# Kernel optimization log

Measured on AMD Instinct MI355X. Metric: run time of the kernel, lower is better.

Reference implementation:

```python
import jax, jax.numpy as jnp
import numpy as np

H = 64        # hidden_size
G = 64        # global_hidden_size
VOCAB = 128   # VOCAB_SIZE
NUM_OPS = 20
DEPTH = 12    # complete binary tree: 2**DEPTH - 1 nodes
B = 128       # batch of trees
TEMP = 3.0    # self.temperature


def setup_inputs() -> dict:
    key = jax.random.key(0)
    ks = jax.random.split(key, 16)
    s = 0.05
    N = 2 ** DEPTH - 1
    inp = {
        "x_idx": jax.random.randint(ks[0], (B, N), 0, VOCAB, dtype=jnp.int32),
        "validity_mask": jnp.ones((NUM_OPS,), jnp.float32),
        # binary tree-LSTM (blstm): x one-hot -> gates [i, f_a, f_b, o, u]
        "Wx": jax.random.normal(ks[1], (VOCAB, 5 * H), jnp.float32) * s,
        "Ua": jax.random.normal(ks[2], (H, 5 * H), jnp.float32) * s,
        "Ub": jax.random.normal(ks[3], (H, 5 * H), jnp.float32) * s,
        "b_tree": jnp.zeros((5 * H,), jnp.float32),
        # global nn.LSTM (1 layer), gate order i,f,g,o
        "W_ih": jax.random.normal(ks[4], (H, 4 * G), jnp.float32) * s,
        "W_hh": jax.random.normal(ks[5], (G, 4 * G), jnp.float32) * s,
        "b_lstm": jnp.zeros((4 * G,), jnp.float32),
        # FFN on root hidden
        "W1": jax.random.normal(ks[6], (H, H), jnp.float32) * s,
        "b1": jnp.zeros((H,), jnp.float32),
        "W2": jax.random.normal(ks[7], (H, H), jnp.float32) * s,
        "b2": jnp.zeros((H,), jnp.float32),
        # actor head on [hidden ; global_hidden]
        "actor_W": jax.random.normal(ks[8], (H + G, NUM_OPS), jnp.float32) * s,
        "actor_b": jnp.zeros((NUM_OPS,), jnp.float32),
    }
    return inp


def _tree_lstm_sweep(x_idx, Wx, Ua, Ub, b_tree):
    """Bottom-up binary tree-LSTM over a complete binary tree.
    Node i's children sit at flat positions 2i+1, 2i+2 (level layout)."""
    h_prev = c_prev = None
    for d in range(DEPTH - 1, -1, -1):
        n = 2 ** d
        off = n - 1
        # memory-bound gather of gate pre-activations: [B, n, 5H]
        z = Wx[x_idx[:, off:off + n]] + b_tree
        if h_prev is not None:
            h_a, h_b = h_prev[:, 0::2], h_prev[:, 1::2]
            c_a, c_b = c_prev[:, 0::2], c_prev[:, 1::2]
            z = z + jnp.einsum("bnh,hg->bng", h_a, Ua) + jnp.einsum("bnh,hg->bng", h_b, Ub)
        i, fa, fb, o, u = jnp.split(z, 5, axis=-1)
        c = jax.nn.sigmoid(i) * jnp.tanh(u)
        if h_prev is not None:
            c = c + jax.nn.sigmoid(fa) * c_a + jax.nn.sigmoid(fb) * c_b
        h = jax.nn.sigmoid(o) * jnp.tanh(c)
        h_prev, c_prev = h, c
    return h_prev[:, 0]  # root hidden [B, H]


def reference(x_idx, validity_mask, Wx, Ua, Ub, b_tree, W_ih, W_hh, b_lstm,
              W1, b1, W2, b2, actor_W, actor_b):
    h_root = _tree_lstm_sweep(x_idx, Wx, Ua, Ub, b_tree)
    # internal op 1: apply_ffn then apply_global_lstm
    f = jnp.maximum(h_root @ W1 + b1, 0.0) @ W2 + b2          # FFN [B, H]
    h0 = jnp.zeros((f.shape[0], G), f.dtype)
    g = f @ W_ih + h0 @ W_hh + b_lstm                          # one LSTM step
    i, fg, gg, o = jnp.split(g, 4, axis=-1)                    # torch order i,f,g,o
    c_g = jax.nn.sigmoid(i) * jnp.tanh(gg)                     # c0 = 0
    h_g = jax.nn.sigmoid(o) * jnp.tanh(c_g)                    # [B, G]
    # external actor with validity-masked weights (as in policy())
    feats = jnp.concatenate([f, h_g], axis=-1)                 # [B, H+G]
    logits = jnp.log(validity_mask) + feats @ (actor_W * validity_mask) + actor_b * validity_mask
    return jax.nn.softmax(logits / TEMP, axis=-1)              # [B, NUM_OPS]
```

## Files before the change

kernel.cpp:

```cpp
#include <hip/hip_runtime.h>


typedef unsigned short u16;
typedef unsigned int   u32;
typedef __attribute__((ext_vector_type(8))) short  short8;
typedef __attribute__((ext_vector_type(4))) float  floatx4;

__device__ __forceinline__ float fsig(float x) {
    return __fdividef(1.0f, 1.0f + __expf(-x));
}
__device__ __forceinline__ float ftanh(float x) {
    return 1.0f - __fdividef(2.0f, __expf(2.0f * x) + 1.0f);
}
__device__ __forceinline__ u16 f2bf(float x) {
    u32 u = __float_as_uint(x);
    return (u16)((u + 0x7FFFu + ((u >> 16) & 1u)) >> 16);
}
__device__ __forceinline__ float bf2f(short s) {
    return __uint_as_float(((u32)(u16)s) << 16);
}
__device__ __forceinline__ float c_from_slots(short lo, short hi) {
    return __uint_as_float((u32)(u16)lo | (((u32)(u16)hi) << 16));
}

#define HS 72
#define CS 65

__global__ void precompute_kernel(
    const float* __restrict__ Wx, const float* __restrict__ b_tree,
    const float* __restrict__ Ua, const float* __restrict__ Ub,
    u16* __restrict__ Wp, u16* __restrict__ Tap, u16* __restrict__ Tbp,
    u16* __restrict__ Uswz)
{
    int v = blockIdx.x;
    int t = threadIdx.x;
    __shared__ float sz[320], sta[320], stb[320], sh[64], sc[64];
    float z = Wx[v * 320 + t] + b_tree[t];
    sz[t] = z;
    {
        int f = v * 320 + t;
        int j = f & 7, lane = (f >> 3) & 63, tk = f >> 9;
        int nt = tk % 20, kc = tk / 20;
        int k = kc * 32 + (lane >> 4) * 8 + j;
        int nn = nt * 16 + (lane & 15);
        float uval = (k < 64) ? Ua[k * 320 + nn] : Ub[(k - 64) * 320 + nn];
        Uswz[f] = f2bf(uval);
    }
    __syncthreads();
    if (t < 64) {
        float c = fsig(sz[t]) * ftanh(sz[256 + t]);
        float h = fsig(sz[192 + t]) * ftanh(c);
        sc[t] = c; sh[t] = h;
    }
    __syncthreads();
    float ta = 0.f, tb = 0.f;
    #pragma unroll
    for (int k = 0; k < 64; ++k) {
        ta += sh[k] * Ua[k * 320 + t];
        tb += sh[k] * Ub[k * 320 + t];
    }
    sta[t] = ta; stb[t] = tb;
    __syncthreads();
    if (t < 64) {
        int hh = t;
        u32 cbits = __float_as_uint(sc[hh]);
        short8 wp, tp, bp;
        #pragma unroll
        for (int g = 0; g < 5; ++g) {
            wp[g] = (short)f2bf(sz[g * 64 + hh]);
            tp[g] = (short)f2bf(sta[g * 64 + hh]);
            bp[g] = (short)f2bf(stb[g * 64 + hh]);
        }
        wp[5] = 0; wp[6] = 0; wp[7] = 0;
        tp[5] = (short)(cbits & 0xFFFF); tp[6] = (short)(cbits >> 16); tp[7] = 0;
        bp[5] = tp[5]; bp[6] = tp[6]; bp[7] = 0;
        *(short8*)(Wp  + ((size_t)v * 64 + hh) * 8) = wp;
        *(short8*)(Tap + ((size_t)v * 64 + hh) * 8) = tp;
        *(short8*)(Tbp + ((size_t)v * 64 + hh) * 8) = bp;
    }
}

template<int MT>
__device__ __forceinline__ void sweep_level(
    const u16* hsrc, const float* csrc,
    u16* hdst, float* cdst,
    u16* hg, float* cg,
    float* hroot,
    const short8 Bfrag[4][5],
    const u16* __restrict__ Wp, const int* __restrict__ xb,
    int nrows, int i0, int loff,
    int lane15, int quad, int wv)
{
    floatx4 acc[MT][5];
    #pragma unroll
    for (int mt = 0; mt < MT; ++mt)
        #pragma unroll
        for (int g = 0; g < 5; ++g) acc[mt][g] = (floatx4){0.f, 0.f, 0.f, 0.f};

    #pragma unroll
    for (int mt = 0; mt < MT; ++mt) {
        #pragma unroll
        for (int kc = 0; kc < 4; ++kc) {
            int child = 2 * (mt * 16 + lane15) + (kc >> 1);
            short8 a = *(const short8*)(hsrc + child * HS + (kc & 1) * 32 + quad * 8);
            #pragma unroll
            for (int g = 0; g < 5; ++g)
                acc[mt][g] = __builtin_amdgcn_mfma_f32_16x16x32_bf16(
                    a, Bfrag[kc][g], acc[mt][g], 0, 0, 0);
        }
    }

    int hh = wv * 16 + lane15;
    #pragma unroll
    for (int mt = 0; mt < MT; ++mt) {
        #pragma unroll
        for (int r = 0; r < 4; ++r) {
            int row = mt * 16 + quad * 4 + r;
            bool valid = row < nrows;
            int id = xb[loff + i0 + row];
            short8 wp = *(const short8*)(Wp + (((size_t)id << 6) + hh) * 8);
            float zi  = acc[mt][0][r] + bf2f(wp[0]);
            float zfa = acc[mt][1][r] + bf2f(wp[1]);
            float zfb = acc[mt][2][r] + bf2f(wp[2]);
            float zo  = acc[mt][3][r] + bf2f(wp[3]);
            float zu  = acc[mt][4][r] + bf2f(wp[4]);
            float ca = csrc[(2 * row) * CS + hh];
            float cb = csrc[(2 * row + 1) * CS + hh];
            float c = fsig(zi) * ftanh(zu) + fsig(zfa) * ca + fsig(zfb) * cb;
            float h = fsig(zo) * ftanh(c);
            if (valid) {
                if (hdst)  { hdst[row * HS + hh] = f2bf(h); cdst[row * CS + hh] = c; }
                if (hg)    { hg[row * 64 + hh] = f2bf(h);   cg[row * 64 + hh] = c; }
                if (hroot) { hroot[hh] = h; }
            }
        }
    }
}

__device__ __forceinline__ void load_bfrags(short8 Bfrag[4][5],
                                            const u16* __restrict__ Uswz,
                                            int wv, int lane)
{
    #pragma unroll
    for (int kc = 0; kc < 4; ++kc)
        #pragma unroll
        for (int g = 0; g < 5; ++g) {
            int nt = g * 4 + wv;
            Bfrag[kc][g] = *(const short8*)(Uswz + ((kc * 20 + nt) * 64 + lane) * 8);
        }
}

__global__ __launch_bounds__(256, 2) void sweepA_kernel(
    const int* __restrict__ x_idx,
    const u16* __restrict__ Wp, const u16* __restrict__ Tap,
    const u16* __restrict__ Tbp, const u16* __restrict__ Uswz,
    u16* __restrict__ h4, float* __restrict__ c4)
{
    __shared__ u16   hA[64 * HS];
    __shared__ u16   hB[32 * HS];
    __shared__ float cA[64 * CS];
    __shared__ float cB[32 * CS];
    int t = threadIdx.x, lane = t & 63, wv = t >> 6;
    int lane15 = lane & 15, quad = lane >> 4;
    int b = blockIdx.x >> 4, st = blockIdx.x & 15;
    const int* xb = x_idx + b * 4095;

    short8 Bfrag[4][5];
    load_bfrags(Bfrag, Uswz, wv, lane);

    #pragma unroll 2
    for (int rr = 0; rr < 16; ++rr) {
        int rl = wv * 16 + rr;
        int i = st * 64 + rl;
        int id  = xb[1023 + i];
        int ida = xb[2047 + 2 * i];
        int idb = xb[2048 + 2 * i];
        short8 wp = *(const short8*)(Wp  + (((size_t)id)  << 9) + lane * 8);
        short8 ta = *(const short8*)(Tap + (((size_t)ida) << 9) + lane * 8);
        short8 tb = *(const short8*)(Tbp + (((size_t)idb) << 9) + lane * 8);
        float zi  = bf2f(wp[0]) + bf2f(ta[0]) + bf2f(tb[0]);
        float zfa = bf2f(wp[1]) + bf2f(ta[1]) + bf2f(tb[1]);
        float zfb = bf2f(wp[2]) + bf2f(ta[2]) + bf2f(tb[2]);
        float zo  = bf2f(wp[3]) + bf2f(ta[3]) + bf2f(tb[3]);
        float zu  = bf2f(wp[4]) + bf2f(ta[4]) + bf2f(tb[4]);
        float ca = c_from_slots(ta[5], ta[6]);
        float cb = c_from_slots(tb[5], tb[6]);
        float c = fsig(zi) * ftanh(zu) + fsig(zfa) * ca + fsig(zfb) * cb;
        float h = fsig(zo) * ftanh(c);
        hA[rl * HS + lane] = f2bf(h);
        cA[rl * CS + lane] = c;
    }
    __syncthreads();
    sweep_level<2>(hA, cA, hB, cB, nullptr, nullptr, nullptr, Bfrag, Wp, xb,
                   32, st << 5, 511, lane15, quad, wv);
    __syncthreads();
    sweep_level<1>(hB, cB, hA, cA, nullptr, nullptr, nullptr, Bfrag, Wp, xb,
                   16, st << 4, 255, lane15, quad, wv);
    __syncthreads();
    sweep_level<1>(hA, cA, hB, cB, nullptr, nullptr, nullptr, Bfrag, Wp, xb,
                   8, st << 3, 127, lane15, quad, wv);
    __syncthreads();
    sweep_level<1>(hB, cB, hA, cA, nullptr, nullptr, nullptr, Bfrag, Wp, xb,
                   4, st << 2, 63, lane15, quad, wv);
    __syncthreads();
    sweep_level<1>(hA, cA, hB, cB, nullptr, nullptr, nullptr, Bfrag, Wp, xb,
                   2, st << 1, 31, lane15, quad, wv);
    __syncthreads();
    sweep_level<1>(hB, cB, nullptr, nullptr,
                   h4 + (size_t)(b * 16 + st) * 64, c4 + (size_t)(b * 16 + st) * 64,
                   nullptr, Bfrag, Wp, xb, 1, st, 15, lane15, quad, wv);
}

__global__ __launch_bounds__(256, 2) void sweepB_kernel(
    const int* __restrict__ x_idx,
    const u16* __restrict__ Wp, const u16* __restrict__ Uswz,
    const u16* __restrict__ h4, const float* __restrict__ c4,
    const float* __restrict__ W1, const float* __restrict__ b1,
    const float* __restrict__ W2, const float* __restrict__ b2,
    const float* __restrict__ W_ih, const float* __restrict__ b_lstm,
    const float* __restrict__ actor_W, const float* __restrict__ actor_b,
    const float* __restrict__ vm, float* __restrict__ out)
{
    __shared__ u16   hA[32 * HS];
    __shared__ u16   hB[32 * HS];
    __shared__ float cA[32 * CS];
    __shared__ float cB[32 * CS];
    __shared__ float hroot[64];
    int t = threadIdx.x, lane = t & 63, wv = t >> 6;
    int lane15 = lane & 15, quad = lane >> 4;
    int b = blockIdx.x;
    const int* xb = x_idx + b * 4095;

    short8 Bfrag[4][5];
    load_bfrags(Bfrag, Uswz, wv, lane);

    for (int idx = t; idx < 16 * 64; idx += 256) {
        int r = idx >> 6, hh = idx & 63;
        hA[r * HS + hh] = h4[(size_t)(b * 16 + r) * 64 + hh];
        cA[r * CS + hh] = c4[(size_t)(b * 16 + r) * 64 + hh];
    }
    __syncthreads();
    sweep_level<1>(hA, cA, hB, cB, nullptr, nullptr, nullptr, Bfrag, Wp, xb,
                   8, 0, 7, lane15, quad, wv);
    __syncthreads();
    sweep_level<1>(hB, cB, hA, cA, nullptr, nullptr, nullptr, Bfrag, Wp, xb,
                   4, 0, 3, lane15, quad, wv);
    __syncthreads();
    sweep_level<1>(hA, cA, hB, cB, nullptr, nullptr, nullptr, Bfrag, Wp, xb,
                   2, 0, 1, lane15, quad, wv);
    __syncthreads();
    sweep_level<1>(hB, cB, nullptr, nullptr, nullptr, nullptr, hroot, Bfrag, Wp, xb,
                   1, 0, 0, lane15, quad, wv);
    __syncthreads();

    if (wv == 0) {
        float a = b1[lane];
        #pragma unroll 8
        for (int k = 0; k < 64; ++k) a += hroot[k] * W1[k * 64 + lane];
        float r1 = fmaxf(a, 0.f);
        float f = b2[lane];
        #pragma unroll 8
        for (int k = 0; k < 64; ++k) f += __shfl(r1, k) * W2[k * 64 + lane];
        float gi = b_lstm[lane], gg = b_lstm[128 + lane], go = b_lstm[192 + lane];
        #pragma unroll 8
        for (int k = 0; k < 64; ++k) {
            float fk = __shfl(f, k);
            gi += fk * W_ih[k * 256 + lane];
            gg += fk * W_ih[k * 256 + 128 + lane];
            go += fk * W_ih[k * 256 + 192 + lane];
        }
        float cg = fsig(gi) * ftanh(gg);
        float hg = fsig(go) * ftanh(cg);
        int tt = (lane < 20) ? lane : 19;
        float dot = 0.f;
        #pragma unroll 8
        for (int k = 0; k < 64; ++k) {
            float fk = __shfl(f, k), hk = __shfl(hg, k);
            dot += fk * actor_W[k * 20 + tt] + hk * actor_W[(64 + k) * 20 + tt];
        }
        float m = vm[tt];
        float lg = logf(m) + dot * m + actor_b[tt] * m;
        float mx = -1e30f;
        #pragma unroll
        for (int j = 0; j < 20; ++j) mx = fmaxf(mx, __shfl(lg, j));
        float s = 0.f;
        #pragma unroll
        for (int j = 0; j < 20; ++j) s += __expf((__shfl(lg, j) - mx) * (1.0f / 3.0f));
        if (lane < 20) out[b * 20 + lane] = __expf((lg - mx) * (1.0f / 3.0f)) / s;
    }
}

extern "C" void kernel_launch(void* const* d_in, const int* in_sizes, int n_in,
                              void* d_out, int out_size, void* d_ws, size_t ws_size,
                              hipStream_t stream)
{
    const int*   x_idx   = (const int*)d_in[0];
    const float* vm      = (const float*)d_in[1];
    const float* Wx      = (const float*)d_in[2];
    const float* Ua      = (const float*)d_in[3];
    const float* Ub      = (const float*)d_in[4];
    const float* b_tree  = (const float*)d_in[5];
    const float* W_ih    = (const float*)d_in[6];
    const float* b_lstm  = (const float*)d_in[8];
    const float* W1      = (const float*)d_in[9];
    const float* b1      = (const float*)d_in[10];
    const float* W2      = (const float*)d_in[11];
    const float* b2      = (const float*)d_in[12];
    const float* actor_W = (const float*)d_in[13];
    const float* actor_b = (const float*)d_in[14];
    float* out = (float*)d_out;

    float* ws = (float*)d_ws;
    float* c4 = ws;  ws += 2048 * 64;
    u16* u = (u16*)ws;
    u16* Wp   = u;  u += 128 * 64 * 8;
    u16* Tap  = u;  u += 128 * 64 * 8;
    u16* Tbp  = u;  u += 128 * 64 * 8;
    u16* Uswz = u;  u += 128 * 320;
    u16* h4   = u;  u += 2048 * 64;

    precompute_kernel<<<128, 320, 0, stream>>>(Wx, b_tree, Ua, Ub,
                                               Wp, Tap, Tbp, Uswz);
    sweepA_kernel<<<2048, 256, 0, stream>>>(x_idx, Wp, Tap, Tbp, Uswz, h4, c4);
    sweepB_kernel<<<128, 256, 0, stream>>>(x_idx, Wp, Uswz, h4, c4,
                                           W1, b1, W2, b2, W_ih, b_lstm,
                                           actor_W, actor_b, vm, out);
}
```

Before: 183.5 us.

## Rebalance tree sweep split, store cell state in bf16 pairs, use fp32 lookup tables

```diff
diff --git a/kernel.cpp b/kernel.cpp
--- a/kernel.cpp
+++ b/kernel.cpp
@@ -12,24 +12,20 @@
 __device__ __forceinline__ float ftanh(float x) {
     return 1.0f - __fdividef(2.0f, __expf(2.0f * x) + 1.0f);
 }
-__device__ __forceinline__ u16 f2bf(float x) {
-    u32 u = __float_as_uint(x);
-    return (u16)((u + 0x7FFFu + ((u >> 16) & 1u)) >> 16);
-}
-__device__ __forceinline__ float bf2f(short s) {
-    return __uint_as_float(((u32)(u16)s) << 16);
-}
-__device__ __forceinline__ float c_from_slots(short lo, short hi) {
-    return __uint_as_float((u32)(u16)lo | (((u32)(u16)hi) << 16));
-}
+__device__ __forceinline__ u16 f2bfa(float x) {
+    return (u16)((__float_as_uint(x) + 0x8000u) >> 16);
+}
+__device__ __forceinline__ float bflo(u32 cc) { return __uint_as_float(cc << 16); }
+__device__ __forceinline__ float bfhi(u32 cc) { return __uint_as_float(cc & 0xFFFF0000u); }
 
 #define HS 72
-#define CS 65
 
 __global__ void precompute_kernel(
     const float* __restrict__ Wx, const float* __restrict__ b_tree,
     const float* __restrict__ Ua, const float* __restrict__ Ub,
-    u16* __restrict__ Wp, u16* __restrict__ Tap, u16* __restrict__ Tbp,
+    float4* __restrict__ WpA, float* __restrict__ WpU,
+    float4* __restrict__ TaA, float2* __restrict__ TaUC,
+    float4* __restrict__ TbA, float2* __restrict__ TbUC,
     u16* __restrict__ Uswz)
 {
     int v = blockIdx.x;
@@ -44,7 +40,8 @@
         int k = kc * 32 + (lane >> 4) * 8 + j;
         int nn = nt * 16 + (lane & 15);
         float uval = (k < 64) ? Ua[k * 320 + nn] : Ub[(k - 64) * 320 + nn];
-        Uswz[f] = f2bf(uval);
+        Uswz[f] = (u16)((__float_as_uint(uval) + 0x7FFFu +
+                         ((__float_as_uint(uval) >> 16) & 1u)) >> 16);
     }
     __syncthreads();
     if (t < 64) {
@@ -54,7 +51,7 @@
     }
     __syncthreads();
     float ta = 0.f, tb = 0.f;
-    #pragma unroll
+    #pragma unroll 8
     for (int k = 0; k < 64; ++k) {
         ta += sh[k] * Ua[k * 320 + t];
         tb += sh[k] * Ub[k * 320 + t];
@@ -62,46 +59,36 @@
     sta[t] = ta; stb[t] = tb;
     __syncthreads();
     if (t < 64) {
-        int hh = t;
-        u32 cbits = __float_as_uint(sc[hh]);
-        short8 wp, tp, bp;
-        #pragma unroll
-        for (int g = 0; g < 5; ++g) {
-            wp[g] = (short)f2bf(sz[g * 64 + hh]);
-            tp[g] = (short)f2bf(sta[g * 64 + hh]);
-            bp[g] = (short)f2bf(stb[g * 64 + hh]);
-        }
-        wp[5] = 0; wp[6] = 0; wp[7] = 0;
-        tp[5] = (short)(cbits & 0xFFFF); tp[6] = (short)(cbits >> 16); tp[7] = 0;
-        bp[5] = tp[5]; bp[6] = tp[6]; bp[7] = 0;
-        *(short8*)(Wp  + ((size_t)v * 64 + hh) * 8) = wp;
-        *(short8*)(Tap + ((size_t)v * 64 + hh) * 8) = tp;
-        *(short8*)(Tbp + ((size_t)v * 64 + hh) * 8) = bp;
-    }
-}
-
-template<int MT>
+        int o = (v << 6) + t;
+        WpA[o]  = make_float4(sz[t],  sz[64 + t],  sz[128 + t],  sz[192 + t]);
+        WpU[o]  = sz[256 + t];
+        TaA[o]  = make_float4(sta[t], sta[64 + t], sta[128 + t], sta[192 + t]);
+        TaUC[o] = make_float2(sta[256 + t], sc[t]);
+        TbA[o]  = make_float4(stb[t], stb[64 + t], stb[128 + t], stb[192 + t]);
+        TbUC[o] = make_float2(stb[256 + t], sc[t]);
+    }
+}
+
+template<int NT, int MODE>
 __device__ __forceinline__ void sweep_level(
-    const u16* hsrc, const float* csrc,
-    u16* hdst, float* cdst,
-    u16* hg, float* cg,
-    float* hroot,
+    const u16* hsrc, const u16* cps,
+    u16* hdst, u16* cpd, u16* hg, u16* cg, float* hroot,
     const short8 Bfrag[4][5],
-    const u16* __restrict__ Wp, const int* __restrict__ xb,
-    int nrows, int i0, int loff,
+    const float4* __restrict__ WpA, const float* __restrict__ WpU,
+    const int* __restrict__ xb, int loff, int lbase0, int node0,
     int lane15, int quad, int wv)
 {
-    floatx4 acc[MT][5];
+    floatx4 acc[NT][5];
     #pragma unroll
-    for (int mt = 0; mt < MT; ++mt)
+    for (int mt = 0; mt < NT; ++mt)
         #pragma unroll
         for (int g = 0; g < 5; ++g) acc[mt][g] = (floatx4){0.f, 0.f, 0.f, 0.f};
 
     #pragma unroll
-    for (int mt = 0; mt < MT; ++mt) {
+    for (int mt = 0; mt < NT; ++mt) {
         #pragma unroll
         for (int kc = 0; kc < 4; ++kc) {
-            int child = 2 * (mt * 16 + lane15) + (kc >> 1);
+            int child = 2 * (lbase0 + mt * 16 + lane15) + (kc >> 1);
             short8 a = *(const short8*)(hsrc + child * HS + (kc & 1) * 32 + quad * 8);
             #pragma unroll
             for (int g = 0; g < 5; ++g)
@@ -109,29 +96,34 @@
                     a, Bfrag[kc][g], acc[mt][g], 0, 0, 0);
         }
     }
-
     int hh = wv * 16 + lane15;
     #pragma unroll
-    for (int mt = 0; mt < MT; ++mt) {
+    for (int mt = 0; mt < NT; ++mt) {
         #pragma unroll
         for (int r = 0; r < 4; ++r) {
-            int row = mt * 16 + quad * 4 + r;
-            bool valid = row < nrows;
-            int id = xb[loff + i0 + row];
-            short8 wp = *(const short8*)(Wp + (((size_t)id << 6) + hh) * 8);
-            float zi  = acc[mt][0][r] + bf2f(wp[0]);
-            float zfa = acc[mt][1][r] + bf2f(wp[1]);
-            float zfb = acc[mt][2][r] + bf2f(wp[2]);
-            float zo  = acc[mt][3][r] + bf2f(wp[3]);
-            float zu  = acc[mt][4][r] + bf2f(wp[4]);
-            float ca = csrc[(2 * row) * CS + hh];
-            float cb = csrc[(2 * row + 1) * CS + hh];
-            float c = fsig(zi) * ftanh(zu) + fsig(zfa) * ca + fsig(zfb) * cb;
+            int lrow = lbase0 + mt * 16 + quad * 4 + r;
+            int node = node0 + mt * 16 + quad * 4 + r;
+            int id = xb[loff + node];
+            float4 wg = WpA[(id << 6) + hh];
+            float  wu = WpU[(id << 6) + hh];
+            u32 cc = *(const u32*)(cps + lrow * 128 + hh * 2);
+            float zi  = acc[mt][0][r] + wg.x;
+            float zfa = acc[mt][1][r] + wg.y;
+            float zfb = acc[mt][2][r] + wg.z;
+            float zo  = acc[mt][3][r] + wg.w;
+            float zu  = acc[mt][4][r] + wu;
+            float c = fsig(zi) * ftanh(zu) + fsig(zfa) * bflo(cc) + fsig(zfb) * bfhi(cc);
             float h = fsig(zo) * ftanh(c);
-            if (valid) {
-                if (hdst)  { hdst[row * HS + hh] = f2bf(h); cdst[row * CS + hh] = c; }
-                if (hg)    { hg[row * 64 + hh] = f2bf(h);   cg[row * 64 + hh] = c; }
-                if (hroot) { hroot[hh] = h; }
+            if (MODE == 0) {
+                hdst[lrow * HS + hh] = f2bfa(h);
+                cpd[(lrow >> 1) * 128 + hh * 2 + (lrow & 1)] = f2bfa(c);
+            }
+            if (MODE == 1) {
+                hg[node * 64 + hh] = f2bfa(h);
+                cg[(node >> 1) * 128 + hh * 2 + (node & 1)] = f2bfa(c);
+            }
+            if (MODE == 2) {
+                if (lrow == 0) hroot[hh] = h;
             }
         }
     }
@@ -152,105 +144,115 @@
 
 __global__ __launch_bounds__(256, 2) void sweepA_kernel(
     const int* __restrict__ x_idx,
-    const u16* __restrict__ Wp, const u16* __restrict__ Tap,
-    const u16* __restrict__ Tbp, const u16* __restrict__ Uswz,
-    u16* __restrict__ h4, float* __restrict__ c4)
-{
-    __shared__ u16   hA[64 * HS];
-    __shared__ u16   hB[32 * HS];
-    __shared__ float cA[64 * CS];
-    __shared__ float cB[32 * CS];
+    const float4* __restrict__ WpA, const float* __restrict__ WpU,
+    const float4* __restrict__ TaA, const float2* __restrict__ TaUC,
+    const float4* __restrict__ TbA, const float2* __restrict__ TbUC,
+    const u16* __restrict__ Uswz,
+    u16* __restrict__ h7, u16* __restrict__ c7)
+{
+    __shared__ u16 hA[128 * HS];
+    __shared__ u16 cA[64 * 128];
+    __shared__ u16 hB[64 * HS];
+    __shared__ u16 cB[32 * 128];
     int t = threadIdx.x, lane = t & 63, wv = t >> 6;
     int lane15 = lane & 15, quad = lane >> 4;
-    int b = blockIdx.x >> 4, st = blockIdx.x & 15;
+    int b = blockIdx.x >> 3, st = blockIdx.x & 7;
     const int* xb = x_idx + b * 4095;
 
     short8 Bfrag[4][5];
     load_bfrags(Bfrag, Uswz, wv, lane);
 
     #pragma unroll 2
-    for (int rr = 0; rr < 16; ++rr) {
-        int rl = wv * 16 + rr;
-        int i = st * 64 + rl;
+    for (int rr = 0; rr < 32; ++rr) {
+        int rl = wv * 32 + rr;
+        int i = st * 128 + rl;
         int id  = xb[1023 + i];
         int ida = xb[2047 + 2 * i];
         int idb = xb[2048 + 2 * i];
-        short8 wp = *(const short8*)(Wp  + (((size_t)id)  << 9) + lane * 8);
-        short8 ta = *(const short8*)(Tap + (((size_t)ida) << 9) + lane * 8);
-        short8 tb = *(const short8*)(Tbp + (((size_t)idb) << 9) + lane * 8);
-        float zi  = bf2f(wp[0]) + bf2f(ta[0]) + bf2f(tb[0]);
-        float zfa = bf2f(wp[1]) + bf2f(ta[1]) + bf2f(tb[1]);
-        float zfb = bf2f(wp[2]) + bf2f(ta[2]) + bf2f(tb[2]);
-        float zo  = bf2f(wp[3]) + bf2f(ta[3]) + bf2f(tb[3]);
-        float zu  = bf2f(wp[4]) + bf2f(ta[4]) + bf2f(tb[4]);
-        float ca = c_from_slots(ta[5], ta[6]);
-        float cb = c_from_slots(tb[5], tb[6]);
-        float c = fsig(zi) * ftanh(zu) + fsig(zfa) * ca + fsig(zfb) * cb;
+        float4 wg  = WpA[(id  << 6) + lane];
+        float  wu  = WpU[(id  << 6) + lane];
+        float4 tga = TaA[(ida << 6) + lane];
+        float2 tua = TaUC[(ida << 6) + lane];
+        float4 tgb = TbA[(idb << 6) + lane];
+        float2 tub = TbUC[(idb << 6) + lane];
+        float zi  = wg.x + tga.x + tgb.x;
+        float zfa = wg.y + tga.y + tgb.y;
+        float zfb = wg.z + tga.z + tgb.z;
+        float zo  = wg.w + tga.w + tgb.w;
+        float zu  = wu   + tua.x + tub.x;
+        float c = fsig(zi) * ftanh(zu) + fsig(zfa) * tua.y + fsig(zfb) * tub.y;
         float h = fsig(zo) * ftanh(c);
-        hA[rl * HS + lane] = f2bf(h);
-        cA[rl * CS + lane] = c;
-    }
-    __syncthreads();
-    sweep_level<2>(hA, cA, hB, cB, nullptr, nullptr, nullptr, Bfrag, Wp, xb,
-                   32, st << 5, 511, lane15, quad, wv);
-    __syncthreads();
-    sweep_level<1>(hB, cB, hA, cA, nullptr, nullptr, nullptr, Bfrag, Wp, xb,
-                   16, st << 4, 255, lane15, quad, wv);
-    __syncthreads();
-    sweep_level<1>(hA, cA, hB, cB, nullptr, nullptr, nullptr, Bfrag, Wp, xb,
-                   8, st << 3, 127, lane15, quad, wv);
-    __syncthreads();
-    sweep_level<1>(hB, cB, hA, cA, nullptr, nullptr, nullptr, Bfrag, Wp, xb,
-                   4, st << 2, 63, lane15, quad, wv);
-    __syncthreads();
-    sweep_level<1>(hA, cA, hB, cB, nullptr, nullptr, nullptr, Bfrag, Wp, xb,
-                   2, st << 1, 31, lane15, quad, wv);
-    __syncthreads();
-    sweep_level<1>(hB, cB, nullptr, nullptr,
-                   h4 + (size_t)(b * 16 + st) * 64, c4 + (size_t)(b * 16 + st) * 64,
-                   nullptr, Bfrag, Wp, xb, 1, st, 15, lane15, quad, wv);
+        hA[rl * HS + lane] = f2bfa(h);
+        cA[(rl >> 1) * 128 + lane * 2 + (rl & 1)] = f2bfa(c);
+    }
+    __syncthreads();
+    sweep_level<2, 0>(hA, cA, hB, cB, nullptr, nullptr, nullptr, Bfrag, WpA, WpU,
+                      xb, 511, 0,  st * 64,      lane15, quad, wv);
+    sweep_level<2, 0>(hA, cA, hB, cB, nullptr, nullptr, nullptr, Bfrag, WpA, WpU,
+                      xb, 511, 32, st * 64 + 32, lane15, quad, wv);
+    __syncthreads();
+    sweep_level<2, 0>(hB, cB, hA, cA, nullptr, nullptr, nullptr, Bfrag, WpA, WpU,
+                      xb, 255, 0, st * 32, lane15, quad, wv);
+    __syncthreads();
+    sweep_level<1, 1>(hA, cA, nullptr, nullptr,
+                      h7 + (size_t)b * 8192, c7 + (size_t)b * 8192, nullptr,
+                      Bfrag, WpA, WpU, xb, 127, 0, st * 16, lane15, quad, wv);
 }
 
 __global__ __launch_bounds__(256, 2) void sweepB_kernel(
     const int* __restrict__ x_idx,
-    const u16* __restrict__ Wp, const u16* __restrict__ Uswz,
-    const u16* __restrict__ h4, const float* __restrict__ c4,
+    const float4* __restrict__ WpA, const float* __restrict__ WpU,
+    const u16* __restrict__ Uswz,
+    const u16* __restrict__ h7, const u16* __restrict__ c7,
     const float* __restrict__ W1, const float* __restrict__ b1,
     const float* __restrict__ W2, const float* __restrict__ b2,
     const float* __restrict__ W_ih, const float* __restrict__ b_lstm,
     const float* __restrict__ actor_W, const float* __restrict__ actor_b,
     const float* __restrict__ vm, float* __restrict__ out)
 {
-    __shared__ u16   hA[32 * HS];
-    __shared__ u16   hB[32 * HS];
-    __shared__ float cA[32 * CS];
-    __shared__ float cB[32 * CS];
+    __shared__ u16 hA[128 * HS];
+    __shared__ u16 cA[64 * 128];
+    __shared__ u16 hB[64 * HS];
+    __shared__ u16 cB[32 * 128];
     __shared__ float hroot[64];
     int t = threadIdx.x, lane = t & 63, wv = t >> 6;
     int lane15 = lane & 15, quad = lane >> 4;
     int b = blockIdx.x;
     const int* xb = x_idx + b * 4095;
+    const u16* h7b = h7 + (size_t)b * 8192;
+    const u16* c7b = c7 + (size_t)b * 8192;
 
     short8 Bfrag[4][5];
     load_bfrags(Bfrag, Uswz, wv, lane);
 
-    for (int idx = t; idx < 16 * 64; idx += 256) {
-        int r = idx >> 6, hh = idx & 63;
-        hA[r * HS + hh] = h4[(size_t)(b * 16 + r) * 64 + hh];
-        cA[r * CS + hh] = c4[(size_t)(b * 16 + r) * 64 + hh];
-    }
-    __syncthreads();
-    sweep_level<1>(hA, cA, hB, cB, nullptr, nullptr, nullptr, Bfrag, Wp, xb,
-                   8, 0, 7, lane15, quad, wv);
-    __syncthreads();
-    sweep_level<1>(hB, cB, hA, cA, nullptr, nullptr, nullptr, Bfrag, Wp, xb,
-                   4, 0, 3, lane15, quad, wv);
-    __syncthreads();
-    sweep_level<1>(hA, cA, hB, cB, nullptr, nullptr, nullptr, Bfrag, Wp, xb,
-                   2, 0, 1, lane15, quad, wv);
-    __syncthreads();
-    sweep_level<1>(hB, cB, nullptr, nullptr, nullptr, nullptr, hroot, Bfrag, Wp, xb,
-                   1, 0, 0, lane15, quad, wv);
+    for (int idx = t; idx < 4096; idx += 256) {
+        int r = idx >> 5, p2 = (idx & 31) * 2;
+        *(u32*)&hA[r * HS + p2] = *(const u32*)&h7b[r * 64 + p2];
+        *(u32*)&cA[idx * 2] = *(const u32*)&c7b[idx * 2];
+    }
+    __syncthreads();
+    sweep_level<2, 0>(hA, cA, hB, cB, nullptr, nullptr, nullptr, Bfrag, WpA, WpU,
+                      xb, 63, 0, 0, lane15, quad, wv);
+    sweep_level<2, 0>(hA, cA, hB, cB, nullptr, nullptr, nullptr, Bfrag, WpA, WpU,
+                      xb, 63, 32, 32, lane15, quad, wv);
+    __syncthreads();
+    sweep_level<2, 0>(hB, cB, hA, cA, nullptr, nullptr, nullptr, Bfrag, WpA, WpU,
+                      xb, 31, 0, 0, lane15, quad, wv);
+    __syncthreads();
+    sweep_level<1, 0>(hA, cA, hB, cB, nullptr, nullptr, nullptr, Bfrag, WpA, WpU,
+                      xb, 15, 0, 0, lane15, quad, wv);
+    __syncthreads();
+    sweep_level<1, 0>(hB, cB, hA, cA, nullptr, nullptr, nullptr, Bfrag, WpA, WpU,
+                      xb, 7, 0, 0, lane15, quad, wv);
+    __syncthreads();
+    sweep_level<1, 0>(hA, cA, hB, cB, nullptr, nullptr, nullptr, Bfrag, WpA, WpU,
+                      xb, 3, 0, 0, lane15, quad, wv);
+    __syncthreads();
+    sweep_level<1, 0>(hB, cB, hA, cA, nullptr, nullptr, nullptr, Bfrag, WpA, WpU,
+                      xb, 1, 0, 0, lane15, quad, wv);
+    __syncthreads();
+    sweep_level<1, 2>(hA, cA, nullptr, nullptr, nullptr, nullptr, hroot,
+                      Bfrag, WpA, WpU, xb, 0, 0, 0, lane15, quad, wv);
     __syncthreads();
 
     if (wv == 0) {
@@ -310,19 +312,22 @@
     const float* actor_b = (const float*)d_in[14];
     float* out = (float*)d_out;
 
-    float* ws = (float*)d_ws;
-    float* c4 = ws;  ws += 2048 * 64;
-    u16* u = (u16*)ws;
-    u16* Wp   = u;  u += 128 * 64 * 8;
-    u16* Tap  = u;  u += 128 * 64 * 8;
-    u16* Tbp  = u;  u += 128 * 64 * 8;
-    u16* Uswz = u;  u += 128 * 320;
-    u16* h4   = u;  u += 2048 * 64;
+    char* ws = (char*)d_ws;
+    float4* WpA  = (float4*)ws;            ws += 128 * 64 * 16;
+    float4* TaA  = (float4*)ws;            ws += 128 * 64 * 16;
+    float4* TbA  = (float4*)ws;            ws += 128 * 64 * 16;
+    float2* TaUC = (float2*)ws;            ws += 128 * 64 * 8;
+    float2* TbUC = (float2*)ws;            ws += 128 * 64 * 8;
+    float*  WpU  = (float*)ws;             ws += 128 * 64 * 4;
+    u16*    h7   = (u16*)ws;               ws += 128 * 8192 * 2;
+    u16*    c7   = (u16*)ws;               ws += 128 * 8192 * 2;
+    u16*    Uswz = (u16*)ws;               ws += 128 * 320 * 2;
 
     precompute_kernel<<<128, 320, 0, stream>>>(Wx, b_tree, Ua, Ub,
-                                               Wp, Tap, Tbp, Uswz);
-    sweepA_kernel<<<2048, 256, 0, stream>>>(x_idx, Wp, Tap, Tbp, Uswz, h4, c4);
-    sweepB_kernel<<<128, 256, 0, stream>>>(x_idx, Wp, Uswz, h4, c4,
+                                               WpA, WpU, TaA, TaUC, TbA, TbUC, Uswz);
+    sweepA_kernel<<<1024, 256, 0, stream>>>(x_idx, WpA, WpU, TaA, TaUC,
+                                            TbA, TbUC, Uswz, h7, c7);
+    sweepB_kernel<<<128, 256, 0, stream>>>(x_idx, WpA, WpU, Uswz, h7, c7,
                                            W1, b1, W2, b2, W_ih, b_lstm,
                                            actor_W, actor_b, vm, out);
 }
```

After: 182.0 us. Within noise of the previous version (-0.8%).
